# Optimization experiments

Measured on AMD Instinct MI355X. Metric: run time of the kernel, lower is better.

Reference implementation:

```python
import jax, jax.numpy as jnp
import numpy as np

E = 8        # num_experts
K = 2        # top_k
B, S, D, H = 4, 2048, 1024, 2048  # batch, seq, input_size, hidden_size (GLU -> 2H fan-out)


def act_quant(x):
    # per-token 8-bit absmax quantization (BitNet style)
    scale = 127.0 / jnp.clip(jnp.max(jnp.abs(x), axis=-1, keepdims=True), 1e-5)
    return jnp.clip(jnp.round(x * scale), -128, 127) / scale


def weight_quant(w):
    # per-(expert)-tensor 1.58-bit quantization to {-1,0,1}/scale
    scale = 1.0 / jnp.clip(jnp.mean(jnp.abs(w)), 1e-5)
    return jnp.clip(jnp.round(w * scale), -1, 1) / scale


def ste(x, q):
    # straight-through estimator: forward uses q, backward passes grad of x
    return x + jax.lax.stop_gradient(q - x)


def setup_inputs() -> dict:
    key = jax.random.key(0)
    k0, k1, k2, k3 = jax.random.split(key, 4)
    x = jax.random.normal(k0, (B, S, D), jnp.float32)
    w_gate = jax.random.normal(k1, (D, E), jnp.float32) * 0.02   # router (no bias)
    w_in = jax.random.normal(k2, (E, 2 * H, D), jnp.float32) * 0.02   # ParallelExperts1_58b input_linear [E, out, in]
    w_out = jax.random.normal(k3, (E, D, H), jnp.float32) * 0.02      # output_linear [E, out, in]
    bias = jnp.zeros((D,), jnp.float32)
    return {"x": x, "w_gate": w_gate, "w_in": w_in, "w_out": w_out, "bias": bias}


def reference(x, w_gate, w_in, w_out, bias):
    bsz, length, d = x.shape
    xf = x.reshape(-1, d)                               # [N, D]
    logits = xf @ w_gate                                # [N, E]
    top_logits, top_idx = jax.lax.top_k(logits, K)      # [N, K]
    gates = jax.nn.softmax(top_logits, axis=-1)         # [N, K]

    # load-balancing aux loss (switch loss + z-loss), training-mode router loss
    probs = jax.nn.softmax(logits, axis=-1)
    onehot = jax.nn.one_hot(top_idx, E, dtype=logits.dtype).sum(axis=1)  # [N, E]
    freq = onehot.sum(axis=0)
    p = probs.sum(axis=0)
    switchloss = E * jnp.sum((p / jnp.sum(p)) * (freq / jnp.sum(freq)))
    zloss = jnp.sum(jax.nn.logsumexp(logits, axis=-1) ** 2) / xf.shape[0]
    loss = switchloss + 0.1 * zloss

    # STE-quantized activations and per-expert ternary weights
    xq = ste(xf, act_quant(xf))                          # [N, D]
    win_q = jax.vmap(lambda w: ste(w, weight_quant(w)))(w_in)    # [E, 2H, D]
    wout_q = jax.vmap(lambda w: ste(w, weight_quant(w)))(w_out)  # [E, D, H]

    # dense expert loop (E is small/static); gates zero-out non-routed tokens,
    # equivalent to the gather/grouped-GEMM/index_add pipeline in the original.
    y = jnp.zeros_like(xf)
    for e in range(E):
        gate_e = jnp.sum(jnp.where(top_idx == e, gates, 0.0), axis=1)  # [N]
        h = xq @ win_q[e].T                              # [N, 2H]
        h1, g = jnp.split(h, 2, axis=-1)
        h = jax.nn.silu(h1) * g                          # GLU
        hq = ste(h, act_quant(h))
        y = y + gate_e[:, None] * (hq @ wout_q[e].T)     # [N, D]

    y = y.reshape(bsz, length, d) + bias
    return y, loss
```

## Files before the change

kernel.cpp:

```cpp
#include <hip/hip_runtime.h>
#include <math.h>

typedef __attribute__((ext_vector_type(4)))  int   i32x4;
typedef __attribute__((ext_vector_type(16))) int   i32x16;
typedef __attribute__((ext_vector_type(4)))  float f32x4;
typedef __attribute__((ext_vector_type(8)))  unsigned short u16x8;

#define NTOK   8192
#define DIMD   1024
#define HID    2048
#define NEXP   8
#define NPAIR  16384

#define XQ_OFF      0L
#define WQIN_OFF    8388608L
#define WQOUT_OFF   41943040L
#define XG_OFF      58720256L
#define HG_OFF      79691776L
#define GLUG_OFF    121634816L
#define XRECG_OFF   205520896L
#define GATE_OFF    205602816L
#define HRECG_OFF   205668352L
#define TLIST_OFF   205750272L
#define CNT_OFF     206012416L
#define PSUM_OFF    206012448L
#define ZSUM_OFF    206012480L
#define PART_OFF    206012512L
#define WRECIN_OFF  206015616L
#define WRECOUT_OFF 206015648L
#define WSCLIN_OFF  206015680L
#define WSCLOUT_OFF 206015712L
#define OFF_OFF     206015744L

__device__ __forceinline__ int clampi(int v, int lo, int hi){ return v<lo?lo:(v>hi?hi:v); }

__device__ __forceinline__ unsigned packq(f32x4 v, float s, int lo, int hi){
  int q0 = clampi((int)rintf(v.x*s), lo, hi);
  int q1 = clampi((int)rintf(v.y*s), lo, hi);
  int q2 = clampi((int)rintf(v.z*s), lo, hi);
  int q3 = clampi((int)rintf(v.w*s), lo, hi);
  return (unsigned)((q0&255)|((q1&255)<<8)|((q2&255)<<16)|((q3&255)<<24));
}

__device__ __forceinline__ unsigned short f2bf(float f){
  unsigned u = __float_as_uint(f);
  u += 0x7fffu + ((u >> 16) & 1u);
  return (unsigned short)(u >> 16);
}
__device__ __forceinline__ float bf2f(unsigned short b){
  return __uint_as_float(((unsigned)b) << 16);
}

__global__ void k_init(int* __restrict__ cnts, float* __restrict__ psum, float* __restrict__ zsum){
  int i = threadIdx.x;
  if (i < 8){ cnts[i]=0; psum[i]=0.f; }
  if (i == 8) zsum[0]=0.f;
}

__global__ __launch_bounds__(1024) void k_router(
    const float* __restrict__ x, const float* __restrict__ wg,
    signed char* __restrict__ xq, float* __restrict__ xrec,
    float* __restrict__ gatep, int* __restrict__ tlist, int* __restrict__ cnts,
    float* __restrict__ psum, float* __restrict__ zsum)
{
  __shared__ float ls_p[8]; __shared__ float ls_z[1];
  __shared__ int ls_c[8];  __shared__ int ls_b[8];
  int tid = threadIdx.x;
  if (tid<8){ ls_p[tid]=0.f; ls_c[tid]=0; }
  if (tid==8) ls_z[0]=0.f;
  __syncthreads();
  int wave = tid>>6, lane = tid&63;
  int tok = blockIdx.x*16 + wave;

  const f32x4* x4 = (const f32x4*)(x + (long)tok*DIMD) + lane*4;
  f32x4 xv[4];
  #pragma unroll
  for (int j=0;j<4;++j) xv[j] = x4[j];

  float amax = 0.f;
  float lg[8] = {0,0,0,0,0,0,0,0};
  const f32x4* wg4 = (const f32x4*)wg;
  #pragma unroll
  for (int j=0;j<16;++j){
    float xd = xv[j>>2][j&3];
    amax = fmaxf(amax, fabsf(xd));
    int d = lane*16 + j;
    f32x4 w0 = wg4[d*2], w1 = wg4[d*2+1];
    lg[0]+=xd*w0.x; lg[1]+=xd*w0.y; lg[2]+=xd*w0.z; lg[3]+=xd*w0.w;
    lg[4]+=xd*w1.x; lg[5]+=xd*w1.y; lg[6]+=xd*w1.z; lg[7]+=xd*w1.w;
  }
  for (int m=1;m<64;m<<=1){
    amax = fmaxf(amax, __shfl_xor(amax, m));
    #pragma unroll
    for (int e=0;e<8;++e) lg[e] += __shfl_xor(lg[e], m);
  }
  float cm = fmaxf(amax, 1e-5f);
  float sx = 127.f/cm;
  unsigned p0 = packq(xv[0], sx, -128, 127);
  unsigned p1 = packq(xv[1], sx, -128, 127);
  unsigned p2 = packq(xv[2], sx, -128, 127);
  unsigned p3 = packq(xv[3], sx, -128, 127);
  i32x4 pk; pk.x=(int)p0; pk.y=(int)p1; pk.z=(int)p2; pk.w=(int)p3;
  *(i32x4*)(xq + (long)tok*DIMD + lane*16) = pk;

  int e1=0, e2=0, s1=0, s2=0;
  if (lane==0){
    xrec[tok] = cm*(1.f/127.f);
    e1 = 0;
    for (int e=1;e<8;++e) if (lg[e] > lg[e1]) e1 = e;
    e2 = (e1==0)?1:0;
    for (int e=0;e<8;++e) if (e!=e1 && lg[e] > lg[e2]) e2 = e;
    float t = expf(lg[e2]-lg[e1]);
    gatep[tok*2]   = 1.f/(1.f+t);
    gatep[tok*2+1] = t/(1.f+t);
    float mx = lg[e1], sum = 0.f, pr[8];
    #pragma unroll
    for (int e=0;e<8;++e){ pr[e] = expf(lg[e]-mx); sum += pr[e]; }
    float inv = 1.f/sum;
    #pragma unroll
    for (int e=0;e<8;++e) atomicAdd(&ls_p[e], pr[e]*inv);
    float lse = mx + logf(sum);
    atomicAdd(&ls_z[0], lse*lse);
    s1 = atomicAdd(&ls_c[e1], 1);
    s2 = atomicAdd(&ls_c[e2], 1);
  }
  __syncthreads();
  if (tid<8) ls_b[tid] = atomicAdd(&cnts[tid], ls_c[tid]);
  __syncthreads();
  if (lane==0){
    tlist[e1*NTOK + ls_b[e1] + s1] = tok*2;
    tlist[e2*NTOK + ls_b[e2] + s2] = tok*2 + 1;
  }
  if (tid<8)  atomicAdd(&psum[tid], ls_p[tid]);
  if (tid==8) atomicAdd(zsum, ls_z[0]);
}

__global__ void k_wabs(const float* __restrict__ w_in, const float* __restrict__ w_out,
                       float* __restrict__ part){
  int b = blockIdx.x, tid = threadIdx.x;
  const float* base = (b < 512) ? (w_in + (long)b*65536) : (w_out + (long)(b-512)*65536);
  const f32x4* p4 = (const f32x4*)base;
  float s = 0.f;
  for (int i = tid; i < 16384; i += 256){
    f32x4 v = p4[i];
    s += fabsf(v.x)+fabsf(v.y)+fabsf(v.z)+fabsf(v.w);
  }
  __shared__ float red[256];
  red[tid] = s; __syncthreads();
  for (int off=128; off; off>>=1){ if (tid<off) red[tid]+=red[tid+off]; __syncthreads(); }
  if (tid==0) part[b] = red[0];
}

__global__ void k_wmean(const float* __restrict__ part, const int* __restrict__ cnts,
                        float* __restrict__ wrec_in, float* __restrict__ wrec_out,
                        float* __restrict__ wscl_in, float* __restrict__ wscl_out,
                        int* __restrict__ off){
  int t = threadIdx.x;
  if (t < 8){
    float s = 0.f;
    for (int i=0;i<64;++i) s += part[t*64+i];
    float cmm = fmaxf(s/4194304.f, 1e-5f);
    wrec_in[t] = cmm; wscl_in[t] = 1.f/cmm;
  } else if (t < 16){
    int e = t-8; float s = 0.f;
    for (int i=0;i<32;++i) s += part[512 + e*32 + i];
    float cmm = fmaxf(s/2097152.f, 1e-5f);
    wrec_out[e] = cmm; wscl_out[e] = 1.f/cmm;
  } else if (t == 16){
    int acc = 0;
    for (int e=0;e<8;++e){ off[e] = acc; acc += (cnts[e] + 511) & ~511; }
  }
}

__global__ void k_packw(const float* __restrict__ w, i32x4* __restrict__ wq,
                        const float* __restrict__ wscl, int COLS, int K, int KB,
                        long chunksPerE){
  long t = (long)blockIdx.x*blockDim.x + threadIdx.x;
  int e = (int)(t / chunksPerE);
  long r = t - (long)e*chunksPerE;
  int lane = (int)(r & 63);
  long fb = r >> 6;
  int kb = (int)(fb % KB);
  int cb = (int)(fb / KB);
  int col = cb*32 + (lane & 31);
  int k0  = kb*32 + (lane >> 5)*16;
  const f32x4* src = (const f32x4*)(w + ((long)e*COLS + col)*K + k0);
  float s = wscl[e];
  f32x4 v0 = src[0], v1 = src[1], v2 = src[2], v3 = src[3];
  i32x4 o;
  o.x = (int)packq(v0, s, -1, 1);
  o.y = (int)packq(v1, s, -1, 1);
  o.z = (int)packq(v2, s, -1, 1);
  o.w = (int)packq(v3, s, -1, 1);
  wq[t] = o;
}

__global__ void k_gatherx(const signed char* __restrict__ xq, const int* __restrict__ tlist,
                          const int* __restrict__ cnts, const int* __restrict__ off,
                          const float* __restrict__ xrec,
                          signed char* __restrict__ xg, float* __restrict__ xrecg){
  int e = blockIdx.x & 7;
  int cnt = cnts[e];
  int w = threadIdx.x >> 6;
  int c = threadIdx.x & 63;
  int goff = off[e];
  signed char* xb = xg + (long)goff*1024;
  for (int r = (blockIdx.x>>3)*4 + w; r < cnt; r += 2048){
    int pr = tlist[e*NTOK + r];
    if (c == 0) xrecg[goff + r] = xrec[pr>>1];
    i32x4 v = *(const i32x4*)(xq + (long)(pr>>1)*DIMD + c*16);
    int kb = c>>1, lhi = c&1;
    *(i32x4*)(xb + ((long)(r>>5)*32 + kb)*1024 + (lhi*32 + (r&31))*16) = v;
  }
}

#define MF(A,B,C) C = __builtin_amdgcn_mfma_i32_32x32x32_i8(A,B,C,0,0,0)

__global__ __launch_bounds__(512, 4) void k_gemm1(
    const signed char* __restrict__ xg, const signed char* __restrict__ wqin,
    const int* __restrict__ cnts, const int* __restrict__ off,
    const float* __restrict__ xrecg_all, const float* __restrict__ wrec_in,
    unsigned short* __restrict__ glug_all)
{
  __shared__ signed char bsh[65536];
  const int e = blockIdx.x & 7;
  const int ctile = blockIdx.x >> 3;
  const int cnt = cnts[e];
  const int tid = threadIdx.x;
  const int goff = off[e];
  {
    const i32x4* s0 = (const i32x4*)(wqin + (long)e*4194304 + (long)ctile*32768);
    const i32x4* s1 = (const i32x4*)(wqin + (long)e*4194304 + (long)(64+ctile)*32768);
    i32x4* d = (i32x4*)bsh;
    #pragma unroll
    for (int i=0;i<4;++i){ d[tid + i*512] = s0[tid + i*512]; d[2048 + tid + i*512] = s1[tid + i*512]; }
  }
  __syncthreads();

  const int wave = tid>>6, lane = tid&63, l31 = lane&31, lhi = lane>>5;
  const float wr = wrec_in[e];
  const float* xrecg = xrecg_all + goff;
  unsigned short* glug = glug_all + (long)goff*HID;
  const signed char* xbase = xg + (long)goff*1024;
  const signed char* lb = bsh + lane*16;
  const int maxit = (cnt + 511) >> 9;

  #pragma unroll 1
  for (int it=0; it<maxit; ++it){
    const int rb = it*512 + wave*64;
    const i32x4* a0 = (const i32x4*)(xbase + (long)(rb>>5)*32768) + lane;
    const i32x4* a1 = a0 + 2048;

    i32x16 p0=(i32x16)0, p1=(i32x16)0, q0=(i32x16)0, q1=(i32x16)0;
    i32x4 eA0=a0[0], eA1=a1[0];
    i32x4 oA0=a0[64], oA1=a1[64];
    i32x4 eB0=*(const i32x4*)(lb),      eB1=*(const i32x4*)(lb+32768);
    i32x4 oB0=*(const i32x4*)(lb+1024), oB1=*(const i32x4*)(lb+33792);
    #pragma unroll 1
    for (int kb=0; kb<30; kb+=2){
      a0+=128; a1+=128;
      MF(eA0,eB0,p0); MF(eA1,eB0,p1); MF(eA0,eB1,q0); MF(eA1,eB1,q1);
      eA0=a0[0]; eA1=a1[0];
      eB0=*(const i32x4*)(lb + (kb+2)*1024);
      eB1=*(const i32x4*)(lb + 32768 + (kb+2)*1024);
      MF(oA0,oB0,p0); MF(oA1,oB0,p1); MF(oA0,oB1,q0); MF(oA1,oB1,q1);
      oA0=a0[64]; oA1=a1[64];
      oB0=*(const i32x4*)(lb + (kb+3)*1024);
      oB1=*(const i32x4*)(lb + 32768 + (kb+3)*1024);
    }
    MF(eA0,eB0,p0); MF(eA1,eB0,p1); MF(eA0,eB1,q0); MF(eA1,eB1,q1);
    MF(oA0,oB0,p0); MF(oA1,oB0,p1); MF(oA0,oB1,q0); MF(oA1,oB1,q1);

#define GLUEPI(P,Q,ROFF) { \
    _Pragma("unroll") \
    for (int g=0; g<16; ++g){ \
      int r = rb + ROFF + (g&3) + 8*(g>>2) + 4*lhi; \
      if (r < cnt){ \
        float dq = xrecg[r]*wr; \
        float h1 = (float)P[g]*dq; \
        float gg = (float)Q[g]*dq; \
        float t = __expf(-h1); \
        float v = h1*gg*__builtin_amdgcn_rcpf(1.f+t); \
        glug[(long)r*HID + ctile*32 + l31] = f2bf(v); \
      } \
    } }
    GLUEPI(p0,q0,0)
    GLUEPI(p1,q1,32)
#undef GLUEPI
  }
}

__global__ __launch_bounds__(256) void k_quanthg(
    const unsigned short* __restrict__ glug, const int* __restrict__ tlist,
    const int* __restrict__ cnts, const int* __restrict__ off,
    const float* __restrict__ gatep, signed char* __restrict__ hg, float* __restrict__ hrecg){
  int e = blockIdx.x & 7;
  int cnt = cnts[e];
  const int wv = threadIdx.x>>6, lane = threadIdx.x&63;
  int r = (blockIdx.x>>3)*4 + wv;
  if (r >= cnt) return;
  const int* tl = tlist + e*NTOK;
  int goff = off[e];
  signed char* hb = hg + (long)goff*2048;
  const unsigned short* row = glug + (long)(goff+r)*HID;

  u16x8 v0 = *(const u16x8*)(row + lane*8);
  u16x8 v1 = *(const u16x8*)(row + 512 + lane*8);
  u16x8 v2 = *(const u16x8*)(row + 1024 + lane*8);
  u16x8 v3 = *(const u16x8*)(row + 1536 + lane*8);
  float m = 0.f;
  #pragma unroll
  for (int j=0;j<8;++j){
    m = fmaxf(m, fmaxf(fmaxf(fabsf(bf2f(v0[j])), fabsf(bf2f(v1[j]))),
                       fmaxf(fabsf(bf2f(v2[j])), fabsf(bf2f(v3[j])))));
  }
  #pragma unroll
  for (int mm=1; mm<64; mm<<=1) m = fmaxf(m, __shfl_xor(m, mm));
  float cmm = fmaxf(m, 1e-5f);
  if (lane == 0) hrecg[goff + r] = gatep[tl[r]] * cmm * (1.f/127.f);
  float s = 127.f/cmm;

#define QCHUNK(V, CIDX) { \
    f32x4 a, b; \
    a.x=bf2f(V[0]); a.y=bf2f(V[1]); a.z=bf2f(V[2]); a.w=bf2f(V[3]); \
    b.x=bf2f(V[4]); b.y=bf2f(V[5]); b.z=bf2f(V[6]); b.w=bf2f(V[7]); \
    uint2 u; u.x = packq(a, s, -128, 127); u.y = packq(b, s, -128, 127); \
    int c = (CIDX); \
    int kb = c>>2, lhi = (c>>1)&1, h = c&1; \
    *(uint2*)(hb + ((long)(r>>5)*64 + kb)*1024 + (lhi*32 + (r&31))*16 + h*8) = u; \
  }
  QCHUNK(v0, lane)
  QCHUNK(v1, lane+64)
  QCHUNK(v2, lane+128)
  QCHUNK(v3, lane+192)
#undef QCHUNK
}

__global__ __launch_bounds__(512, 4) void k_gemm2(
    const signed char* __restrict__ hg, const signed char* __restrict__ wqout,
    const int* __restrict__ tlist, const int* __restrict__ cnts, const int* __restrict__ off,
    const float* __restrict__ hrecg_all, const float* __restrict__ wrec_out,
    unsigned short* __restrict__ pout)
{
  __shared__ signed char bsh[65536];
  const int e = blockIdx.x & 7;
  const int j = blockIdx.x >> 3;
  const int ctile = j & 31;
  const int rh = j >> 5;
  const int cnt = cnts[e];
  const int tid = threadIdx.x;
  const int goff = off[e];
  {
    const i32x4* s0 = (const i32x4*)(wqout + (long)e*2097152 + (long)ctile*65536);
    i32x4* d = (i32x4*)bsh;
    #pragma unroll
    for (int i=0;i<8;++i) d[tid + i*512] = s0[tid + i*512];
  }
  __syncthreads();

  const int wave = tid>>6, lane = tid&63, l31 = lane&31, lhi = lane>>5;
  const int* tl = tlist + e*NTOK;
  const float wr = wrec_out[e];
  const float* hrecg = hrecg_all + goff;
  const signed char* hbase = hg + (long)goff*2048;
  const signed char* lb = bsh + lane*16;
  const int maxit = (cnt + 1023) >> 10;

  #pragma unroll 1
  for (int it=rh; it<maxit; it+=2){
    const int rb = it*1024 + wave*128;
    const i32x4* a0 = (const i32x4*)(hbase + (long)(rb>>5)*65536) + lane;
    const i32x4* a1 = a0 + 4096;
    const i32x4* a2 = a0 + 8192;
    const i32x4* a3 = a0 + 12288;

    i32x16 c0=(i32x16)0, c1=(i32x16)0, c2=(i32x16)0, c3=(i32x16)0;
    i32x4 eA0=a0[0], eA1=a1[0], eA2=a2[0], eA3=a3[0];
    i32x4 oA0=a0[64], oA1=a1[64], oA2=a2[64], oA3=a3[64];
    i32x4 eB=*(const i32x4*)(lb);
    i32x4 oB=*(const i32x4*)(lb+1024);
    #pragma unroll 1
    for (int kb=0; kb<62; kb+=2){
      a0+=128; a1+=128; a2+=128; a3+=128;
      MF(eA0,eB,c0); MF(eA1,eB,c1); MF(eA2,eB,c2); MF(eA3,eB,c3);
      eA0=a0[0]; eA1=a1[0]; eA2=a2[0]; eA3=a3[0];
      eB=*(const i32x4*)(lb + (kb+2)*1024);
      MF(oA0,oB,c0); MF(oA1,oB,c1); MF(oA2,oB,c2); MF(oA3,oB,c3);
      oA0=a0[64]; oA1=a1[64]; oA2=a2[64]; oA3=a3[64];
      oB=*(const i32x4*)(lb + (kb+3)*1024);
    }
    MF(eA0,eB,c0); MF(eA1,eB,c1); MF(eA2,eB,c2); MF(eA3,eB,c3);
    MF(oA0,oB,c0); MF(oA1,oB,c1); MF(oA2,oB,c2); MF(oA3,oB,c3);

#define OUTEPI(C,ROFF) { \
    _Pragma("unroll") \
    for (int g=0; g<16; ++g){ \
      int r = rb + ROFF + (g&3) + 8*(g>>2) + 4*lhi; \
      if (r < cnt){ \
        int pr = tl[r]; \
        float f = hrecg[r]*wr; \
        pout[(long)pr*DIMD + ctile*32 + l31] = f2bf((float)C[g]*f); \
      } \
    } }
    OUTEPI(c0,0)
    OUTEPI(c1,32)
    OUTEPI(c2,64)
    OUTEPI(c3,96)
#undef OUTEPI
  }
}

__global__ void k_combine(const unsigned short* __restrict__ pout, const float* __restrict__ bias,
                          float* __restrict__ y){
  long idx = (long)blockIdx.x*blockDim.x + threadIdx.x;
  int tok = (int)(idx >> 7);
  int c8  = (int)(idx & 127);
  u16x8 pa = ((const u16x8*)(pout + (long)tok*2*DIMD))[c8];
  u16x8 pb = ((const u16x8*)(pout + (long)tok*2*DIMD + DIMD))[c8];
  const f32x4* b4 = (const f32x4*)(bias) + c8*2;
  f32x4 b0 = b4[0], b1 = b4[1];
  f32x4 r0, r1;
  r0.x = b0.x + bf2f(pa[0]) + bf2f(pb[0]);
  r0.y = b0.y + bf2f(pa[1]) + bf2f(pb[1]);
  r0.z = b0.z + bf2f(pa[2]) + bf2f(pb[2]);
  r0.w = b0.w + bf2f(pa[3]) + bf2f(pb[3]);
  r1.x = b1.x + bf2f(pa[4]) + bf2f(pb[4]);
  r1.y = b1.y + bf2f(pa[5]) + bf2f(pb[5]);
  r1.z = b1.z + bf2f(pa[6]) + bf2f(pb[6]);
  r1.w = b1.w + bf2f(pa[7]) + bf2f(pb[7]);
  f32x4* yp = (f32x4*)(y + (long)tok*DIMD) + c8*2;
  yp[0] = r0; yp[1] = r1;
}

__global__ void k_loss(const int* __restrict__ cnts, const float* __restrict__ psum,
                       const float* __restrict__ zsum, float* __restrict__ out){
  if (threadIdx.x==0 && blockIdx.x==0){
    float sp=0.f, sf=0.f, sw=0.f;
    for (int e=0;e<8;++e){
      float f = (float)cnts[e];
      sp += psum[e]; sf += f; sw += psum[e]*f;
    }
    float loss = 8.f*sw/(sp*sf) + 0.1f*zsum[0]/(float)NTOK;
    out[(long)NTOK*DIMD] = loss;
  }
}

extern "C" void kernel_launch(void* const* d_in, const int* in_sizes, int n_in,
                              void* d_out, int out_size, void* d_ws, size_t ws_size,
                              hipStream_t stream){
  const float* x     = (const float*)d_in[0];
  const float* wg    = (const float*)d_in[1];
  const float* w_in  = (const float*)d_in[2];
  const float* w_out = (const float*)d_in[3];
  const float* bias  = (const float*)d_in[4];
  float* y = (float*)d_out;
  char* ws = (char*)d_ws;

  signed char* xq    = (signed char*)(ws + XQ_OFF);
  signed char* wqin  = (signed char*)(ws + WQIN_OFF);
  signed char* wqout = (signed char*)(ws + WQOUT_OFF);
  signed char* xg    = (signed char*)(ws + XG_OFF);
  signed char* hg    = (signed char*)(ws + HG_OFF);
  unsigned short* glug = (unsigned short*)(ws + GLUG_OFF);
  unsigned short* pout = (unsigned short*)(ws + GLUG_OFF);
  float* xrecg = (float*)(ws + XRECG_OFF);
  float* gatep = (float*)(ws + GATE_OFF);
  float* hrecg = (float*)(ws + HRECG_OFF);
  int* tlist = (int*)(ws + TLIST_OFF);
  int* cnts  = (int*)(ws + CNT_OFF);
  float* psum = (float*)(ws + PSUM_OFF);
  float* zsum = (float*)(ws + ZSUM_OFF);
  float* part = (float*)(ws + PART_OFF);
  float* wrec_in  = (float*)(ws + WRECIN_OFF);
  float* wrec_out = (float*)(ws + WRECOUT_OFF);
  float* wscl_in  = (float*)(ws + WSCLIN_OFF);
  float* wscl_out = (float*)(ws + WSCLOUT_OFF);
  int* offe = (int*)(ws + OFF_OFF);

  float* xrec = (float*)(ws + HRECG_OFF);

  k_init  <<<1, 64, 0, stream>>>(cnts, psum, zsum);
  k_router<<<512, 1024, 0, stream>>>(x, wg, xq, xrec, gatep, tlist, cnts, psum, zsum);
  k_wabs  <<<768, 256, 0, stream>>>(w_in, w_out, part);
  k_wmean <<<1, 64, 0, stream>>>(part, cnts, wrec_in, wrec_out, wscl_in, wscl_out, offe);
  k_packw <<<8192, 256, 0, stream>>>(w_in,  (i32x4*)wqin,  wscl_in,  4096, 1024, 32, 262144L);
  k_packw <<<4096, 256, 0, stream>>>(w_out, (i32x4*)wqout, wscl_out, 1024, 2048, 64, 131072L);
  k_gatherx<<<4096, 256, 0, stream>>>(xq, tlist, cnts, offe, xrec, xg, xrecg);
  k_gemm1 <<<512, 512, 0, stream>>>(xg, wqin, cnts, offe, xrecg, wrec_in, glug);
  k_quanthg<<<16384, 256, 0, stream>>>(glug, tlist, cnts, offe, gatep, hg, hrecg);
  k_gemm2 <<<512, 512, 0, stream>>>(hg, wqout, tlist, cnts, offe, hrecg, wrec_out, pout);
  k_combine<<<4096, 256, 0, stream>>>(pout, bias, y);
  k_loss  <<<1, 64, 0, stream>>>(cnts, psum, zsum, y);
}
```

Baseline: 392.9 us.

## Double per-block weight tile in both expert GEMMs using 128KB dynamic LDS

Both grouped int8 GEMMs now stage a weight tile twice as wide in LDS (128KB, dynamic shared memory) and run 1024-thread blocks, with half as many blocks. Each wave now covers fewer rows but more output columns, so a single A fragment feeds more MFMAs and each block reads the activation rows once for twice the columns. The aim is to cut global re-reads of activations across column tiles. The cost is lower occupancy (one block per CU because of the LDS size), more LDS reads per MFMA for B, and fewer blocks to spread over the CUs.

```diff
diff --git a/kernel.cpp b/kernel.cpp
--- a/kernel.cpp
+++ b/kernel.cpp
@@ -216,24 +216,29 @@
 
 #define MF(A,B,C) C = __builtin_amdgcn_mfma_i32_32x32x32_i8(A,B,C,0,0,0)
 
-__global__ __launch_bounds__(512, 4) void k_gemm1(
+__global__ __launch_bounds__(1024, 4) void k_gemm1(
     const signed char* __restrict__ xg, const signed char* __restrict__ wqin,
     const int* __restrict__ cnts, const int* __restrict__ off,
     const float* __restrict__ xrecg_all, const float* __restrict__ wrec_in,
     unsigned short* __restrict__ glug_all)
 {
-  __shared__ signed char bsh[65536];
+  extern __shared__ signed char bsh[];
   const int e = blockIdx.x & 7;
-  const int ctile = blockIdx.x >> 3;
+  const int ct = blockIdx.x >> 3;
   const int cnt = cnts[e];
   const int tid = threadIdx.x;
   const int goff = off[e];
   {
-    const i32x4* s0 = (const i32x4*)(wqin + (long)e*4194304 + (long)ctile*32768);
-    const i32x4* s1 = (const i32x4*)(wqin + (long)e*4194304 + (long)(64+ctile)*32768);
+    const long eb = (long)e*4194304;
+    const i32x4* s0 = (const i32x4*)(wqin + eb + (long)(ct*2      )*32768);
+    const i32x4* s1 = (const i32x4*)(wqin + eb + (long)(ct*2 +  1 )*32768);
+    const i32x4* s2 = (const i32x4*)(wqin + eb + (long)(ct*2 + 64 )*32768);
+    const i32x4* s3 = (const i32x4*)(wqin + eb + (long)(ct*2 + 65 )*32768);
     i32x4* d = (i32x4*)bsh;
-    #pragma unroll
-    for (int i=0;i<4;++i){ d[tid + i*512] = s0[tid + i*512]; d[2048 + tid + i*512] = s1[tid + i*512]; }
+    d[tid]        = s0[tid]; d[tid+1024]        = s0[tid+1024];
+    d[2048 + tid] = s1[tid]; d[2048 + tid+1024] = s1[tid+1024];
+    d[4096 + tid] = s2[tid]; d[4096 + tid+1024] = s2[tid+1024];
+    d[6144 + tid] = s3[tid]; d[6144 + tid+1024] = s3[tid+1024];
   }
   __syncthreads();
 
@@ -247,41 +252,45 @@
 
   #pragma unroll 1
   for (int it=0; it<maxit; ++it){
-    const int rb = it*512 + wave*64;
+    const int rb = it*512 + wave*32;
     const i32x4* a0 = (const i32x4*)(xbase + (long)(rb>>5)*32768) + lane;
-    const i32x4* a1 = a0 + 2048;
 
     i32x16 p0=(i32x16)0, p1=(i32x16)0, q0=(i32x16)0, q1=(i32x16)0;
-    i32x4 eA0=a0[0], eA1=a1[0];
-    i32x4 oA0=a0[64], oA1=a1[64];
-    i32x4 eB0=*(const i32x4*)(lb),      eB1=*(const i32x4*)(lb+32768);
-    i32x4 oB0=*(const i32x4*)(lb+1024), oB1=*(const i32x4*)(lb+33792);
+    i32x4 eA=a0[0], oA=a0[64];
+    i32x4 eB0=*(const i32x4*)(lb),       eB1=*(const i32x4*)(lb+32768);
+    i32x4 eB2=*(const i32x4*)(lb+65536), eB3=*(const i32x4*)(lb+98304);
+    i32x4 oB0=*(const i32x4*)(lb+1024),       oB1=*(const i32x4*)(lb+32768+1024);
+    i32x4 oB2=*(const i32x4*)(lb+65536+1024), oB3=*(const i32x4*)(lb+98304+1024);
     #pragma unroll 1
     for (int kb=0; kb<30; kb+=2){
-      a0+=128; a1+=128;
-      MF(eA0,eB0,p0); MF(eA1,eB0,p1); MF(eA0,eB1,q0); MF(eA1,eB1,q1);
-      eA0=a0[0]; eA1=a1[0];
+      a0 += 128;
+      MF(eA,eB0,p0); MF(eA,eB1,p1); MF(eA,eB2,q0); MF(eA,eB3,q1);
+      eA = a0[0];
       eB0=*(const i32x4*)(lb + (kb+2)*1024);
       eB1=*(const i32x4*)(lb + 32768 + (kb+2)*1024);
-      MF(oA0,oB0,p0); MF(oA1,oB0,p1); MF(oA0,oB1,q0); MF(oA1,oB1,q1);
-      oA0=a0[64]; oA1=a1[64];
+      eB2=*(const i32x4*)(lb + 65536 + (kb+2)*1024);
+      eB3=*(const i32x4*)(lb + 98304 + (kb+2)*1024);
+      MF(oA,oB0,p0); MF(oA,oB1,p1); MF(oA,oB2,q0); MF(oA,oB3,q1);
+      oA = a0[64];
       oB0=*(const i32x4*)(lb + (kb+3)*1024);
       oB1=*(const i32x4*)(lb + 32768 + (kb+3)*1024);
+      oB2=*(const i32x4*)(lb + 65536 + (kb+3)*1024);
+      oB3=*(const i32x4*)(lb + 98304 + (kb+3)*1024);
     }
-    MF(eA0,eB0,p0); MF(eA1,eB0,p1); MF(eA0,eB1,q0); MF(eA1,eB1,q1);
-    MF(oA0,oB0,p0); MF(oA1,oB0,p1); MF(oA0,oB1,q0); MF(oA1,oB1,q1);
-
-#define GLUEPI(P,Q,ROFF) { \
+    MF(eA,eB0,p0); MF(eA,eB1,p1); MF(eA,eB2,q0); MF(eA,eB3,q1);
+    MF(oA,oB0,p0); MF(oA,oB1,p1); MF(oA,oB2,q0); MF(oA,oB3,q1);
+
+#define GLUEPI(P,Q,CO) { \
     _Pragma("unroll") \
     for (int g=0; g<16; ++g){ \
-      int r = rb + ROFF + (g&3) + 8*(g>>2) + 4*lhi; \
+      int r = rb + (g&3) + 8*(g>>2) + 4*lhi; \
       if (r < cnt){ \
         float dq = xrecg[r]*wr; \
         float h1 = (float)P[g]*dq; \
         float gg = (float)Q[g]*dq; \
         float t = __expf(-h1); \
         float v = h1*gg*__builtin_amdgcn_rcpf(1.f+t); \
-        glug[(long)r*HID + ctile*32 + l31] = f2bf(v); \
+        glug[(long)r*HID + ct*64 + (CO) + l31] = f2bf(v); \
       } \
     } }
     GLUEPI(p0,q0,0)
@@ -336,25 +345,29 @@
 #undef QCHUNK
 }
 
-__global__ __launch_bounds__(512, 4) void k_gemm2(
+__global__ __launch_bounds__(1024, 4) void k_gemm2(
     const signed char* __restrict__ hg, const signed char* __restrict__ wqout,
     const int* __restrict__ tlist, const int* __restrict__ cnts, const int* __restrict__ off,
     const float* __restrict__ hrecg_all, const float* __restrict__ wrec_out,
     unsigned short* __restrict__ pout)
 {
-  __shared__ signed char bsh[65536];
+  extern __shared__ signed char bsh[];
   const int e = blockIdx.x & 7;
-  const int j = blockIdx.x >> 3;
-  const int ctile = j & 31;
-  const int rh = j >> 5;
+  const int ct = (blockIdx.x >> 3) & 15;
+  const int rh = blockIdx.x >> 7;
   const int cnt = cnts[e];
   const int tid = threadIdx.x;
   const int goff = off[e];
   {
-    const i32x4* s0 = (const i32x4*)(wqout + (long)e*2097152 + (long)ctile*65536);
+    const long eb = (long)e*2097152;
+    const i32x4* s0 = (const i32x4*)(wqout + eb + (long)(ct*2    )*65536);
+    const i32x4* s1 = (const i32x4*)(wqout + eb + (long)(ct*2 + 1)*65536);
     i32x4* d = (i32x4*)bsh;
     #pragma unroll
-    for (int i=0;i<8;++i) d[tid + i*512] = s0[tid + i*512];
+    for (int i=0;i<4;++i){
+      d[tid + i*1024]        = s0[tid + i*1024];
+      d[4096 + tid + i*1024] = s1[tid + i*1024];
+    }
   }
   __syncthreads();
 
@@ -368,44 +381,44 @@
 
   #pragma unroll 1
   for (int it=rh; it<maxit; it+=2){
-    const int rb = it*1024 + wave*128;
+    const int rb = it*1024 + wave*64;
     const i32x4* a0 = (const i32x4*)(hbase + (long)(rb>>5)*65536) + lane;
     const i32x4* a1 = a0 + 4096;
-    const i32x4* a2 = a0 + 8192;
-    const i32x4* a3 = a0 + 12288;
-
-    i32x16 c0=(i32x16)0, c1=(i32x16)0, c2=(i32x16)0, c3=(i32x16)0;
-    i32x4 eA0=a0[0], eA1=a1[0], eA2=a2[0], eA3=a3[0];
-    i32x4 oA0=a0[64], oA1=a1[64], oA2=a2[64], oA3=a3[64];
-    i32x4 eB=*(const i32x4*)(lb);
-    i32x4 oB=*(const i32x4*)(lb+1024);
+
+    i32x16 c00=(i32x16)0, c01=(i32x16)0, c10=(i32x16)0, c11=(i32x16)0;
+    i32x4 eA0=a0[0], eA1=a1[0];
+    i32x4 oA0=a0[64], oA1=a1[64];
+    i32x4 eB0=*(const i32x4*)(lb),      eB1=*(const i32x4*)(lb+65536);
+    i32x4 oB0=*(const i32x4*)(lb+1024), oB1=*(const i32x4*)(lb+65536+1024);
     #pragma unroll 1
     for (int kb=0; kb<62; kb+=2){
-      a0+=128; a1+=128; a2+=128; a3+=128;
-      MF(eA0,eB,c0); MF(eA1,eB,c1); MF(eA2,eB,c2); MF(eA3,eB,c3);
-      eA0=a0[0]; eA1=a1[0]; eA2=a2[0]; eA3=a3[0];
-      eB=*(const i32x4*)(lb + (kb+2)*1024);
-      MF(oA0,oB,c0); MF(oA1,oB,c1); MF(oA2,oB,c2); MF(oA3,oB,c3);
-      oA0=a0[64]; oA1=a1[64]; oA2=a2[64]; oA3=a3[64];
-      oB=*(const i32x4*)(lb + (kb+3)*1024);
+      a0+=128; a1+=128;
+      MF(eA0,eB0,c00); MF(eA0,eB1,c01); MF(eA1,eB0,c10); MF(eA1,eB1,c11);
+      eA0=a0[0]; eA1=a1[0];
+      eB0=*(const i32x4*)(lb + (kb+2)*1024);
+      eB1=*(const i32x4*)(lb + 65536 + (kb+2)*1024);
+      MF(oA0,oB0,c00); MF(oA0,oB1,c01); MF(oA1,oB0,c10); MF(oA1,oB1,c11);
+      oA0=a0[64]; oA1=a1[64];
+      oB0=*(const i32x4*)(lb + (kb+3)*1024);
+      oB1=*(const i32x4*)(lb + 65536 + (kb+3)*1024);
     }
-    MF(eA0,eB,c0); MF(eA1,eB,c1); MF(eA2,eB,c2); MF(eA3,eB,c3);
-    MF(oA0,oB,c0); MF(oA1,oB,c1); MF(oA2,oB,c2); MF(oA3,oB,c3);
-
-#define OUTEPI(C,ROFF) { \
+    MF(eA0,eB0,c00); MF(eA0,eB1,c01); MF(eA1,eB0,c10); MF(eA1,eB1,c11);
+    MF(oA0,oB0,c00); MF(oA0,oB1,c01); MF(oA1,oB0,c10); MF(oA1,oB1,c11);
+
+#define OUTEPI(C,RO,CO) { \
     _Pragma("unroll") \
     for (int g=0; g<16; ++g){ \
-      int r = rb + ROFF + (g&3) + 8*(g>>2) + 4*lhi; \
+      int r = rb + (RO) + (g&3) + 8*(g>>2) + 4*lhi; \
       if (r < cnt){ \
         int pr = tl[r]; \
         float f = hrecg[r]*wr; \
-        pout[(long)pr*DIMD + ctile*32 + l31] = f2bf((float)C[g]*f); \
+        pout[(long)pr*DIMD + ct*64 + (CO) + l31] = f2bf((float)C[g]*f); \
       } \
     } }
-    OUTEPI(c0,0)
-    OUTEPI(c1,32)
-    OUTEPI(c2,64)
-    OUTEPI(c3,96)
+    OUTEPI(c00,0,0)
+    OUTEPI(c01,0,32)
+    OUTEPI(c10,32,0)
+    OUTEPI(c11,32,32)
 #undef OUTEPI
   }
 }
@@ -479,6 +492,9 @@
 
   float* xrec = (float*)(ws + HRECG_OFF);
 
+  hipFuncSetAttribute((const void*)k_gemm1, hipFuncAttributeMaxDynamicSharedMemorySize, 131072);
+  hipFuncSetAttribute((const void*)k_gemm2, hipFuncAttributeMaxDynamicSharedMemorySize, 131072);
+
   k_init  <<<1, 64, 0, stream>>>(cnts, psum, zsum);
   k_router<<<512, 1024, 0, stream>>>(x, wg, xq, xrec, gatep, tlist, cnts, psum, zsum);
   k_wabs  <<<768, 256, 0, stream>>>(w_in, w_out, part);
@@ -486,9 +502,9 @@
   k_packw <<<8192, 256, 0, stream>>>(w_in,  (i32x4*)wqin,  wscl_in,  4096, 1024, 32, 262144L);
   k_packw <<<4096, 256, 0, stream>>>(w_out, (i32x4*)wqout, wscl_out, 1024, 2048, 64, 131072L);
   k_gatherx<<<4096, 256, 0, stream>>>(xq, tlist, cnts, offe, xrec, xg, xrecg);
-  k_gemm1 <<<512, 512, 0, stream>>>(xg, wqin, cnts, offe, xrecg, wrec_in, glug);
+  k_gemm1 <<<256, 1024, 131072, stream>>>(xg, wqin, cnts, offe, xrecg, wrec_in, glug);
   k_quanthg<<<16384, 256, 0, stream>>>(glug, tlist, cnts, offe, gatep, hg, hrecg);
-  k_gemm2 <<<512, 512, 0, stream>>>(hg, wqout, tlist, cnts, offe, hrecg, wrec_out, pout);
+  k_gemm2 <<<256, 1024, 131072, stream>>>(hg, wqout, tlist, cnts, offe, hrecg, wrec_out, pout);
   k_combine<<<4096, 256, 0, stream>>>(pout, bias, y);
   k_loss  <<<1, 64, 0, stream>>>(cnts, psum, zsum, y);
 }
```

After: 428.7 us. 9.1% more time.
